# Kernel optimization log

Hardware: AMD Instinct MI355X
Metric: run time of the kernel (lower is better)

Reference implementation:

```python
import jax, jax.numpy as jnp
import numpy as np

SEQ_LEN, BATCH, T = 128, 32, 32
START, END = 30, 31  # start_tag / end_tag from init_kwargs


def setup_inputs() -> dict:
    key = jax.random.key(0)
    k1, k2 = jax.random.split(key)
    scores = jax.random.normal(k1, (SEQ_LEN, BATCH, T, T, T), dtype=jnp.float32)
    target = jax.random.randint(k2, (SEQ_LEN, BATCH, 1), 0, T ** 3, dtype=jnp.int64)
    mask = jnp.ones((SEQ_LEN, BATCH), dtype=bool)
    return {"scores": scores, "target": target, "mask": mask}


def reference(scores, target, mask):
    seq_len, bat = scores.shape[0], scores.shape[1]

    # gold-path energy: gather flattened tag-triple score at each step, masked sum
    flat = scores.reshape(seq_len, bat, -1)                  # (S, B, T^3)
    tg = jnp.take_along_axis(flat, target, axis=2)[..., 0]   # (S, B)
    tg_energy = jnp.sum(jnp.where(mask, tg, jnp.zeros((), tg.dtype)))

    # init partition over (prev_prev=START fixed out) -> (B, T, T) over (prev, cur)
    p1 = scores[0, :, START, START, :]                       # (B, T)
    partition = p1[:, :, None] + scores[1, :, START, :, :]   # (B, T, T)

    # forward-algorithm recurrence: logsumexp out oldest tag each step
    def step(part, inp):
        s_t, m_t = inp                                       # (B,T,T,T), (B,)
        cur = s_t + part[:, :, :, None]                      # broadcast over new tag
        cp = jax.nn.logsumexp(cur, axis=1)                   # (B, T, T)
        part = jnp.where(m_t[:, None, None], cp, part)
        return part, None

    partition, _ = jax.lax.scan(step, partition, (scores[2:], mask[2:]))

    z = partition[:, END, END].sum()
    return (z - tg_energy) / bat  # average_batch=True
```

## Files before the change

kernel.cpp:

```cpp
#include <hip/hip_runtime.h>
#include <hip/hip_bf16.h>
#include <math.h>

#define SEQ_LEN 128
#define BATCH   32
#define T       32
#define TT      (T*T)
#define TTT     (T*T*T)
#define START   30
#define END     31

#define LOG2E   1.44269504088896f
#define OFF4    5.77078016355587f

typedef unsigned long long u64;

__device__ __forceinline__ u64 pt_pack(int tag, float v) {
    union { float f; unsigned int u; } c; c.f = v;
    return ((u64)(unsigned int)tag << 32) | (u64)c.u;
}
__device__ __forceinline__ float pt_val(u64 w) {
    union { unsigned int u; float f; } c; c.u = (unsigned int)w; return c.f;
}
__device__ __forceinline__ int pt_tag(u64 w) { return (int)(w >> 32); }

__device__ __forceinline__ u64 ald64(const u64* p) {
    return __hip_atomic_load(p, __ATOMIC_RELAXED, __HIP_MEMORY_SCOPE_AGENT);
}
__device__ __forceinline__ void ast64(u64* p, u64 v) {
    __hip_atomic_store(p, v, __ATOMIC_RELAXED, __HIP_MEMORY_SCOPE_AGENT);
}

#define BLOCK_SYNC() do {                                   \
    asm volatile("s_waitcnt lgkmcnt(0)" ::: "memory");      \
    __builtin_amdgcn_sched_barrier(0);                      \
    __builtin_amdgcn_s_barrier();                           \
    __builtin_amdgcn_sched_barrier(0);                      \
} while (0)

__global__ __launch_bounds__(256) void tg_kernel(const float* __restrict__ scores,
                                                 const int*   __restrict__ target,
                                                 const int*   __restrict__ mask,
                                                 float*       __restrict__ ws) {
    int idx = blockIdx.x * 256 + threadIdx.x;
    float v = 0.0f;
    if (mask[idx] != 0) v = scores[(size_t)idx * TTT + target[idx]];
    #pragma unroll
    for (int off = 32; off > 0; off >>= 1) v += __shfl_down(v, off, 64);
    __shared__ float partial[4];
    int wave = threadIdx.x >> 6, lane = threadIdx.x & 63;
    if (lane == 0) partial[wave] = v;
    __syncthreads();
    if (threadIdx.x == 0)
        ws[blockIdx.x] = partial[0] + partial[1] + partial[2] + partial[3];
}

__global__ __launch_bounds__(256) void init_dfb(const float* __restrict__ scores,
                                                u64* __restrict__ ptF,
                                                u64* __restrict__ ptB) {
    const int blk = blockIdx.x, tid = threadIdx.x;
    if (blk < BATCH) {
        const int b = blk;
        u64* pt = ptF + (size_t)b * 2048;
        #pragma unroll
        for (int q = 0; q < 4; ++q) {
            int e = q * 256 + tid;
            int i = e & 31, j = e >> 5;
            float p1 = scores[(size_t)(0*BATCH + b)*TTT + START*TT + START*T + i];
            float s1 = scores[(size_t)(1*BATCH + b)*TTT + START*TT + i*T + j];
            pt[1024 + e] = pt_pack(1, __expf(p1 + s1));
            pt[e]        = 0ULL;
        }
    } else {
        const int b = blk - BATCH;
        u64* pt = ptB + (size_t)b * 2048;
        #pragma unroll
        for (int q = 0; q < 4; ++q) {
            int e = q * 256 + tid;
            float v = (e == END*T + END) ? 1.0f : 0.0f;
            pt[e]        = pt_pack(128, v);
            pt[1024 + e] = 0ULL;
        }
    }
}

__global__ __launch_bounds__(512, 4) void scan_rd(const float* __restrict__ scores,
                                                  const int*   __restrict__ maskI,
                                                  u64*         __restrict__ ptF,
                                                  u64*         __restrict__ ptB) {
    const int bid   = blockIdx.x;
    const int g     = bid & 7;
    const int chain = bid >> 3;
    const int b     = chain & 31;
    const bool dirB = (chain >> 5) != 0;
    const int tid   = threadIdx.x;
    const int lane  = tid & 63;

    const u64 mlo = __ballot(maskI[lane * BATCH + b] != 0);
    const u64 mhi = __ballot(maskI[(64 + lane) * BATCH + b] != 0);
    auto act_of = [&](int t) {
        return (((t < 64) ? (mlo >> t) : (mhi >> (t - 64))) & 1ULL) != 0ULL;
    };

    u64* const pt = (dirB ? ptB : ptF) + (size_t)b * 2048;
    const int i0 = tid >> 5;
    const int f  = tid & 31;
    const size_t offA = (size_t)i0 * TT + g * 128 + f * 4;
    auto sb = [&](int t) { return scores + ((size_t)t * BATCH + b) * TTT; };

    if (!dirB) {
        __shared__ __align__(16) float sm[4][128 * 33];
        __shared__ __align__(16) float pld[2][128];
        const int oF = tid >> 2, s4 = tid & 3;
        const int jj = oF >> 5, k = oF & 31;
        const int jcol = 4 * g + jj;
        const int ownW = k * 32 + jcol;
        float lastval = pt_val(pt[1024 + ownW]);

        float4 X0, X1;
        auto issue = [&](int t) {
            const float* p = sb(t) + offA;
            X0 = *(const float4*)p; X1 = *(const float4*)(p + 16 * TT);
        };
        auto scat = [&](int bf) {
            #pragma unroll
            for (int q = 0; q < 4; ++q) {
                sm[bf][(f*4 + q)*33 + i0]      = (&X0.x)[q];
                sm[bf][(f*4 + q)*33 + i0 + 16] = (&X1.x)[q];
            }
        };

        issue(2); scat(2);
        issue(3); scat(3);
        issue(4);
        __syncthreads();

        for (int t = 2; t <= 64; ++t) {
            const bool act  = act_of(t);
            const int  pbuf = t & 1;
            if (t + 2 <= 64) scat((t + 2) & 3);
            if (t + 3 <= 64) issue(t + 3);
            if (tid < 64) {
                const int tagw = t - 1;
                const u64* src = pt + (size_t)((t - 1) & 1) * 1024 + 128 * g;
                u64 w0, w1; bool d0 = false, d1 = false;
                for (;;) {
                    if (!d0) { w0 = ald64(src + lane);      d0 = pt_tag(w0) == tagw; }
                    if (!d1) { w1 = ald64(src + 64 + lane); d1 = pt_tag(w1) == tagw; }
                    if (__all(d0 && d1)) break;
                }
                pld[pbuf][lane]      = pt_val(w0);
                pld[pbuf][lane + 64] = pt_val(w1);
            }
            BLOCK_SYNC();
            u64* dst = pt + (size_t)(t & 1) * 1024;
            if (act) {
                const float* row = &sm[t & 3][oF * 33 + 8 * s4];
                const float* pp  = &pld[pbuf][jj * 32 + 8 * s4];
                float acc = 0.f;
                #pragma unroll
                for (int m = 0; m < 8; ++m)
                    acc = fmaf(exp2f(fmaf(row[m], LOG2E, -OFF4)), pp[m], acc);
                acc += __shfl_xor(acc, 1, 64);
                acc += __shfl_xor(acc, 2, 64);
                if (s4 == 0) { lastval = acc; ast64(dst + ownW, pt_pack(t, acc)); }
            } else {
                if (s4 == 0) ast64(dst + ownW, pt_pack(t, lastval));
            }
        }
    } else {
        __shared__ __align__(16) float pld[2][128];
        const int jj = f >> 3, k4 = f & 7;
        const int jb = 4 * g + jj;
        const int ownW0 = i0 * 32 + jb, ownW1 = (i0 + 16) * 32 + jb;
        float last0 = pt_val(pt[ownW0]);
        float last1 = pt_val(pt[ownW1]);

        float4 A0, A1, B0, B1;
        auto issueR = [&](float4& Y0, float4& Y1, int t) {
            const float* p = sb(t) + offA;
            Y0 = *(const float4*)p; Y1 = *(const float4*)(p + 16 * TT);
        };

        auto stepB = [&](int t, const float4& X0, const float4& X1) {
            const bool act  = act_of(t);
            const int  pbuf = t & 1;
            if (tid < 64) {
                const int tagw = t + 1;
                const u64* src = pt + (size_t)((t + 1) & 1) * 1024 + 128 * g;
                u64 w0, w1; bool d0 = false, d1 = false;
                for (;;) {
                    if (!d0) { w0 = ald64(src + lane);      d0 = pt_tag(w0) == tagw; }
                    if (!d1) { w1 = ald64(src + 64 + lane); d1 = pt_tag(w1) == tagw; }
                    if (__all(d0 && d1)) break;
                }
                pld[pbuf][lane]      = pt_val(w0);
                pld[pbuf][lane + 64] = pt_val(w1);
            }
            BLOCK_SYNC();
            u64* dst = pt + (size_t)(t & 1) * 1024;
            if (act) {
                const float4 Rv = *(const float4*)&pld[pbuf][jj * 32 + 4 * k4];
                float a0, a1;
                a0 = exp2f(fmaf(X0.x, LOG2E, -OFF4)) * Rv.x;
                a0 = fmaf(exp2f(fmaf(X0.y, LOG2E, -OFF4)), Rv.y, a0);
                a0 = fmaf(exp2f(fmaf(X0.z, LOG2E, -OFF4)), Rv.z, a0);
                a0 = fmaf(exp2f(fmaf(X0.w, LOG2E, -OFF4)), Rv.w, a0);
                a1 = exp2f(fmaf(X1.x, LOG2E, -OFF4)) * Rv.x;
                a1 = fmaf(exp2f(fmaf(X1.y, LOG2E, -OFF4)), Rv.y, a1);
                a1 = fmaf(exp2f(fmaf(X1.z, LOG2E, -OFF4)), Rv.z, a1);
                a1 = fmaf(exp2f(fmaf(X1.w, LOG2E, -OFF4)), Rv.w, a1);
                a0 += __shfl_xor(a0, 1, 64); a0 += __shfl_xor(a0, 2, 64); a0 += __shfl_xor(a0, 4, 64);
                a1 += __shfl_xor(a1, 1, 64); a1 += __shfl_xor(a1, 2, 64); a1 += __shfl_xor(a1, 4, 64);
                if (k4 == 0) {
                    last0 = a0; last1 = a1;
                    ast64(dst + ownW0, pt_pack(t, a0));
                    ast64(dst + ownW1, pt_pack(t, a1));
                }
            } else {
                if (k4 == 0) {
                    ast64(dst + ownW0, pt_pack(t, last0));
                    ast64(dst + ownW1, pt_pack(t, last1));
                }
            }
        };

        issueR(A0, A1, 127);
        for (int t = 127; t >= 65; t -= 2) {
            if (t - 1 >= 65) issueR(B0, B1, t - 1);
            stepB(t, A0, A1);
            if (t - 2 >= 65) issueR(A0, A1, t - 2);
            if (t - 1 >= 65) stepB(t - 1, B0, B1);
        }
    }
}

__global__ __launch_bounds__(1024) void finalize_dfb(const float* __restrict__ ws,
                                                     const u64*  __restrict__ ptF,
                                                     const u64*  __restrict__ ptB,
                                                     const int*  __restrict__ mask,
                                                     float*      __restrict__ out) {
    __shared__ float zs[32];
    const int w = threadIdx.x >> 6, lane = threadIdx.x & 63;
    for (int rep = 0; rep < 2; ++rep) {
        const int b = w + rep * 16;
        const u64* qf = ptF + (size_t)b * 2048;
        const u64* rb = ptB + (size_t)b * 2048 + 1024;
        float dot = 0.f;
        #pragma unroll
        for (int e = 0; e < 16; ++e) {
            const int x = lane + 64 * e;
            dot += pt_val(qf[x]) * pt_val(rb[(x & 31) * 32 + (x >> 5)]);
        }
        float cnt = 0.f;
        {
            int t = 2 + lane;
            if (t < SEQ_LEN) cnt += (mask[t*BATCH + b] != 0) ? 1.f : 0.f;
            t += 64;
            if (t < SEQ_LEN) cnt += (mask[t*BATCH + b] != 0) ? 1.f : 0.f;
        }
        #pragma unroll
        for (int off = 32; off > 0; off >>= 1) {
            dot += __shfl_xor(dot, off, 64);
            cnt += __shfl_xor(cnt, off, 64);
        }
        if (lane == 0) zs[b] = 4.0f * cnt + logf(dot);
    }
    __syncthreads();
    if (threadIdx.x == 0) {
        float tg = 0.f, z = 0.f;
        #pragma unroll
        for (int i = 0; i < 16; ++i) tg += ws[i];
        #pragma unroll
        for (int i = 0; i < 32; ++i) z += zs[i];
        out[0] = (z - tg) / (float)BATCH;
    }
}

__global__ __launch_bounds__(1024) void scan_fast(const float* __restrict__ scores,
                                                  const int*   __restrict__ maskI,
                                                  float*       __restrict__ ws) {
    const int b    = blockIdx.x;
    const int tid  = threadIdx.x;
    const int w    = tid >> 6;
    const int lane = tid & 63;
    const int h    = lane >> 4;
    const int jp   = (lane >> 3) & 1;
    const int k4   = lane & 7;
    const int j    = w * 2 + jp;

    __shared__ float Q[2][TT];
    __shared__ int   lmask[SEQ_LEN];
    if (tid < SEQ_LEN) lmask[tid] = maskI[tid * BATCH + b];
    {
        int x = tid >> 5, y = tid & 31;
        float p1 = scores[(size_t)(0*BATCH + b)*TTT + START*TT + START*T + x];
        float s1 = scores[(size_t)(1*BATCH + b)*TTT + START*TT + x*T + y];
        Q[1][x*T + y] = __expf(p1 + s1);
    }
    __syncthreads();
    const int loff = h*8*TT + j*T + k4*4;
    float4 SA[8], SB[8];
    auto issue = [&](float4 (&S)[8], int t) {
        const float* p = scores + ((size_t)t*BATCH + b)*TTT + loff;
        #pragma unroll
        for (int m = 0; m < 8; ++m) S[m] = *(const float4*)(p + m*TT);
    };
    auto process = [&](float4 (&S)[8], int t) {
        const float* qc = Q[(t-1) & 1];
        float*       qn = Q[t & 1];
        #pragma unroll
        for (int m = 0; m < 8; ++m) {
            S[m].x = exp2f(fmaf(S[m].x, LOG2E, -OFF4));
            S[m].y = exp2f(fmaf(S[m].y, LOG2E, -OFF4));
            S[m].z = exp2f(fmaf(S[m].z, LOG2E, -OFF4));
            S[m].w = exp2f(fmaf(S[m].w, LOG2E, -OFF4));
        }
        float4 acc = make_float4(0.f, 0.f, 0.f, 0.f);
        #pragma unroll
        for (int m = 0; m < 8; ++m) {
            float q = qc[(h*8 + m)*T + j];
            acc.x = fmaf(S[m].x, q, acc.x);
            acc.y = fmaf(S[m].y, q, acc.y);
            acc.z = fmaf(S[m].z, q, acc.z);
            acc.w = fmaf(S[m].w, q, acc.w);
        }
        acc.x += __shfl_xor(acc.x, 16, 64); acc.y += __shfl_xor(acc.y, 16, 64);
        acc.z += __shfl_xor(acc.z, 16, 64); acc.w += __shfl_xor(acc.w, 16, 64);
        acc.x += __shfl_xor(acc.x, 32, 64); acc.y += __shfl_xor(acc.y, 32, 64);
        acc.z += __shfl_xor(acc.z, 32, 64); acc.w += __shfl_xor(acc.w, 32, 64);
        if (lane < 16) {
            if (lmask[t] != 0) *(float4*)&qn[j*T + k4*4] = acc;
            else               *(float4*)&qn[j*T + k4*4] = *(const float4*)&qc[j*T + k4*4];
        }
        asm volatile("s_waitcnt lgkmcnt(0)" ::: "memory");
        __builtin_amdgcn_s_barrier();
    };
    issue(SA, 2);
    for (int t = 2; t < SEQ_LEN; t += 2) {
        issue(SB, t + 1);
        process(SA, t);
        if (t + 2 < SEQ_LEN) issue(SA, t + 2);
        process(SB, t + 1);
    }
    if (tid == 0) {
        int cnt = 0;
        for (int t = 2; t < SEQ_LEN; ++t) cnt += (lmask[t] != 0);
        ws[16 + b] = 4.0f * (float)cnt + logf(Q[1][END*T + END]);
    }
}

__global__ void finalize_simple(const float* __restrict__ ws, float* __restrict__ out) {
    if (threadIdx.x == 0) {
        float tg = 0.f, z = 0.f;
        #pragma unroll
        for (int i = 0; i < 16; ++i) tg += ws[i];
        #pragma unroll
        for (int i = 0; i < 32; ++i) z += ws[16 + i];
        out[0] = (z - tg) / (float)BATCH;
    }
}

extern "C" void kernel_launch(void* const* d_in, const int* in_sizes, int n_in,
                              void* d_out, int out_size, void* d_ws, size_t ws_size,
                              hipStream_t stream) {
    const float* scores = (const float*)d_in[0];
    const int*   target = (const int*)d_in[1];
    const int*   mask   = (const int*)d_in[2];
    float* out = (float*)d_out;
    float* ws  = (float*)d_ws;
    u64*   ptF = (u64*)((char*)d_ws + 1024);
    u64*   ptB = ptF + (size_t)BATCH * 2048;
    const size_t need = 1024 + (size_t)2 * BATCH * 2048 * sizeof(u64);

    tg_kernel<<<16, 256, 0, stream>>>(scores, target, mask, ws);
    if (ws_size >= need) {
        init_dfb<<<2*BATCH, 256, 0, stream>>>(scores, ptF, ptB);
        scan_rd<<<512, 512, 0, stream>>>(scores, mask, ptF, ptB);
        finalize_dfb<<<1, 1024, 0, stream>>>(ws, ptF, ptB, mask, out);
    } else {
        scan_fast<<<BATCH, 1024, 0, stream>>>(scores, mask, ws);
        finalize_simple<<<1, 64, 0, stream>>>(ws, out);
    }
}
```

Measured before the change: 185.6 us.

## Warp-specialize scan: producer waves prefetch exp'd scores, one consumer wave computes

Restructures the scan kernel into warp-specialized roles. Seven producer waves load scores, apply the exp transform and stage them in a 4-deep LDS ring. A single consumer wave polls the cross-block partition handoff, does the 32-term dot products and publishes results. Block-wide s_barrier syncs are replaced with LDS counters (readyCtr/doneGen) and spin-waits, so loads for future steps overlap the serial chain, and the forward and backward directions share one code path. The cost is that all per-step math lands on one wave, plus the risk of spin contention and ordering bugs under relaxed atomics.

Measured after the change: 200.5 us. +8.0%, slower.

```diff
diff --git a/kernel.cpp b/kernel.cpp
--- a/kernel.cpp
+++ b/kernel.cpp
@@ -9,6 +9,8 @@
 #define TTT     (T*T*T)
 #define START   30
 #define END     31
+#define NGEN    63
+#define TSTR    36
 
 #define LOG2E   1.44269504088896f
 #define OFF4    5.77078016355587f
@@ -31,10 +33,8 @@
     __hip_atomic_store(p, v, __ATOMIC_RELAXED, __HIP_MEMORY_SCOPE_AGENT);
 }
 
-#define BLOCK_SYNC() do {                                   \
+#define LGKM0_FENCE() do {                                  \
     asm volatile("s_waitcnt lgkmcnt(0)" ::: "memory");      \
-    __builtin_amdgcn_sched_barrier(0);                      \
-    __builtin_amdgcn_s_barrier();                           \
     __builtin_amdgcn_sched_barrier(0);                      \
 } while (0)
 
@@ -84,7 +84,7 @@
     }
 }
 
-__global__ __launch_bounds__(512, 4) void scan_rd(const float* __restrict__ scores,
+__global__ __launch_bounds__(512, 4) void scan_w0(const float* __restrict__ scores,
                                                   const int*   __restrict__ maskI,
                                                   u64*         __restrict__ ptF,
                                                   u64*         __restrict__ ptB) {
@@ -96,141 +96,124 @@
     const int tid   = threadIdx.x;
     const int lane  = tid & 63;
 
+    __shared__ __align__(16) float sm[4][128 * TSTR];
+    __shared__ float pldL[128];
+    __shared__ int readyCtr;
+    __shared__ int doneGen;
+
     const u64 mlo = __ballot(maskI[lane * BATCH + b] != 0);
     const u64 mhi = __ballot(maskI[(64 + lane) * BATCH + b] != 0);
     auto act_of = [&](int t) {
         return (((t < 64) ? (mlo >> t) : (mhi >> (t - 64))) & 1ULL) != 0ULL;
     };
 
+    if (tid == 0) { readyCtr = 0; doneGen = -1; }
+    __syncthreads();
+
     u64* const pt = (dirB ? ptB : ptF) + (size_t)b * 2048;
-    const int i0 = tid >> 5;
-    const int f  = tid & 31;
-    const size_t offA = (size_t)i0 * TT + g * 128 + f * 4;
     auto sb = [&](int t) { return scores + ((size_t)t * BATCH + b) * TTT; };
 
-    if (!dirB) {
-        __shared__ __align__(16) float sm[4][128 * 33];
-        __shared__ __align__(16) float pld[2][128];
-        const int oF = tid >> 2, s4 = tid & 3;
-        const int jj = oF >> 5, k = oF & 31;
-        const int jcol = 4 * g + jj;
-        const int ownW = k * 32 + jcol;
-        float lastval = pt_val(pt[1024 + ownW]);
-
-        float4 X0, X1;
-        auto issue = [&](int t) {
-            const float* p = sb(t) + offA;
-            X0 = *(const float4*)p; X1 = *(const float4*)(p + 16 * TT);
-        };
-        auto scat = [&](int bf) {
-            #pragma unroll
-            for (int q = 0; q < 4; ++q) {
-                sm[bf][(f*4 + q)*33 + i0]      = (&X0.x)[q];
-                sm[bf][(f*4 + q)*33 + i0 + 16] = (&X1.x)[q];
+    if (tid >= 64) {
+        const int u = tid - 64;
+        for (int gen = 0; gen < NGEN; ++gen) {
+            const int t = dirB ? (127 - gen) : (2 + gen);
+            if (gen >= 4) {
+                while (__hip_atomic_load(&doneGen, __ATOMIC_RELAXED,
+                                         __HIP_MEMORY_SCOPE_WORKGROUP) < gen - 4) {}
+                asm volatile("" ::: "memory");
+                __builtin_amdgcn_sched_barrier(0);
             }
-        };
-
-        issue(2); scat(2);
-        issue(3); scat(3);
-        issue(4);
-        __syncthreads();
-
-        for (int t = 2; t <= 64; ++t) {
-            const bool act  = act_of(t);
-            const int  pbuf = t & 1;
-            if (t + 2 <= 64) scat((t + 2) & 3);
-            if (t + 3 <= 64) issue(t + 3);
-            if (tid < 64) {
-                const int tagw = t - 1;
-                const u64* src = pt + (size_t)((t - 1) & 1) * 1024 + 128 * g;
-                u64 w0, w1; bool d0 = false, d1 = false;
-                for (;;) {
-                    if (!d0) { w0 = ald64(src + lane);      d0 = pt_tag(w0) == tagw; }
-                    if (!d1) { w1 = ald64(src + 64 + lane); d1 = pt_tag(w1) == tagw; }
-                    if (__all(d0 && d1)) break;
+            const int buf = gen & 3;
+            if (act_of(t)) {
+                const float* base = sb(t);
+                for (int p = u; p < 1024; p += 448) {
+                    const int i = p >> 5;
+                    const int c = p & 31;
+                    float4 v = *(const float4*)(base + (size_t)i * TT + g * 128 + c * 4);
+                    v.x = exp2f(fmaf(v.x, LOG2E, -OFF4));
+                    v.y = exp2f(fmaf(v.y, LOG2E, -OFF4));
+                    v.z = exp2f(fmaf(v.z, LOG2E, -OFF4));
+                    v.w = exp2f(fmaf(v.w, LOG2E, -OFF4));
+                    if (!dirB) {
+                        const int r0 = c * 4;
+                        sm[buf][(r0 + 0) * TSTR + i] = v.x;
+                        sm[buf][(r0 + 1) * TSTR + i] = v.y;
+                        sm[buf][(r0 + 2) * TSTR + i] = v.z;
+                        sm[buf][(r0 + 3) * TSTR + i] = v.w;
+                    } else {
+                        const int row = i * 4 + (c >> 3);
+                        const int col = (c & 7) * 4;
+                        *(float4*)&sm[buf][row * TSTR + col] = v;
+                    }
                 }
-                pld[pbuf][lane]      = pt_val(w0);
-                pld[pbuf][lane + 64] = pt_val(w1);
             }
-            BLOCK_SYNC();
+            LGKM0_FENCE();
+            if (lane == 0)
+                __hip_atomic_fetch_add(&readyCtr, 1, __ATOMIC_RELAXED,
+                                       __HIP_MEMORY_SCOPE_WORKGROUP);
+        }
+    } else {
+        const int o0 = lane, o1 = lane + 64;
+        int w0own, w1own, p0off, p1off;
+        if (!dirB) {
+            const int k = lane & 31;
+            const int jj0 = lane >> 5, jj1 = 2 + (lane >> 5);
+            w0own = k * 32 + 4 * g + jj0;
+            w1own = k * 32 + 4 * g + jj1;
+            p0off = jj0 * 32; p1off = jj1 * 32;
+        } else {
+            w0own = (o0 >> 2) * 32 + 4 * g + (o0 & 3);
+            w1own = (o1 >> 2) * 32 + 4 * g + (o1 & 3);
+            p0off = (o0 & 3) * 32; p1off = (o1 & 3) * 32;
+        }
+        const int parInit = dirB ? 0 : 1;
+        float last0 = pt_val(pt[parInit * 1024 + w0own]);
+        float last1 = pt_val(pt[parInit * 1024 + w1own]);
+
+        for (int gen = 0; gen < NGEN; ++gen) {
+            const int t    = dirB ? (127 - gen) : (2 + gen);
+            const bool act = act_of(t);
+            const int buf  = gen & 3;
+            const int tagw = dirB ? (t + 1) : (t - 1);
+            const int spar = dirB ? ((t + 1) & 1) : ((t - 1) & 1);
+
+            const u64* src = pt + (size_t)spar * 1024 + 128 * g;
+            u64 a0, a1; bool d0 = false, d1 = false;
+            for (;;) {
+                if (!d0) { a0 = ald64(src + lane);      d0 = pt_tag(a0) == tagw; }
+                if (!d1) { a1 = ald64(src + 64 + lane); d1 = pt_tag(a1) == tagw; }
+                if (__all(d0 && d1)) break;
+            }
+
             u64* dst = pt + (size_t)(t & 1) * 1024;
             if (act) {
-                const float* row = &sm[t & 3][oF * 33 + 8 * s4];
-                const float* pp  = &pld[pbuf][jj * 32 + 8 * s4];
-                float acc = 0.f;
+                pldL[lane]      = pt_val(a0);
+                pldL[lane + 64] = pt_val(a1);
+                while (__hip_atomic_load(&readyCtr, __ATOMIC_RELAXED,
+                                         __HIP_MEMORY_SCOPE_WORKGROUP) < 7 * (gen + 1)) {}
+                asm volatile("" ::: "memory");
+                LGKM0_FENCE();
+                const float* e0 = &sm[buf][o0 * TSTR];
+                const float* e1 = &sm[buf][o1 * TSTR];
+                const float* p0 = &pldL[p0off];
+                const float* p1 = &pldL[p1off];
+                float acc0 = 0.f, acc1 = 0.f;
                 #pragma unroll
-                for (int m = 0; m < 8; ++m)
-                    acc = fmaf(exp2f(fmaf(row[m], LOG2E, -OFF4)), pp[m], acc);
-                acc += __shfl_xor(acc, 1, 64);
-                acc += __shfl_xor(acc, 2, 64);
-                if (s4 == 0) { lastval = acc; ast64(dst + ownW, pt_pack(t, acc)); }
+                for (int m = 0; m < 32; ++m) {
+                    acc0 = fmaf(e0[m], p0[m], acc0);
+                    acc1 = fmaf(e1[m], p1[m], acc1);
+                }
+                last0 = acc0; last1 = acc1;
+                ast64(dst + w0own, pt_pack(t, acc0));
+                ast64(dst + w1own, pt_pack(t, acc1));
             } else {
-                if (s4 == 0) ast64(dst + ownW, pt_pack(t, lastval));
+                ast64(dst + w0own, pt_pack(t, last0));
+                ast64(dst + w1own, pt_pack(t, last1));
             }
-        }
-    } else {
-        __shared__ __align__(16) float pld[2][128];
-        const int jj = f >> 3, k4 = f & 7;
-        const int jb = 4 * g + jj;
-        const int ownW0 = i0 * 32 + jb, ownW1 = (i0 + 16) * 32 + jb;
-        float last0 = pt_val(pt[ownW0]);
-        float last1 = pt_val(pt[ownW1]);
-
-        float4 A0, A1, B0, B1;
-        auto issueR = [&](float4& Y0, float4& Y1, int t) {
-            const float* p = sb(t) + offA;
-            Y0 = *(const float4*)p; Y1 = *(const float4*)(p + 16 * TT);
-        };
-
-        auto stepB = [&](int t, const float4& X0, const float4& X1) {
-            const bool act  = act_of(t);
-            const int  pbuf = t & 1;
-            if (tid < 64) {
-                const int tagw = t + 1;
-                const u64* src = pt + (size_t)((t + 1) & 1) * 1024 + 128 * g;
-                u64 w0, w1; bool d0 = false, d1 = false;
-                for (;;) {
-                    if (!d0) { w0 = ald64(src + lane);      d0 = pt_tag(w0) == tagw; }
-                    if (!d1) { w1 = ald64(src + 64 + lane); d1 = pt_tag(w1) == tagw; }
-                    if (__all(d0 && d1)) break;
-                }
-                pld[pbuf][lane]      = pt_val(w0);
-                pld[pbuf][lane + 64] = pt_val(w1);
-            }
-            BLOCK_SYNC();
-            u64* dst = pt + (size_t)(t & 1) * 1024;
-            if (act) {
-                const float4 Rv = *(const float4*)&pld[pbuf][jj * 32 + 4 * k4];
-                float a0, a1;
-                a0 = exp2f(fmaf(X0.x, LOG2E, -OFF4)) * Rv.x;
-                a0 = fmaf(exp2f(fmaf(X0.y, LOG2E, -OFF4)), Rv.y, a0);
-                a0 = fmaf(exp2f(fmaf(X0.z, LOG2E, -OFF4)), Rv.z, a0);
-                a0 = fmaf(exp2f(fmaf(X0.w, LOG2E, -OFF4)), Rv.w, a0);
-                a1 = exp2f(fmaf(X1.x, LOG2E, -OFF4)) * Rv.x;
-                a1 = fmaf(exp2f(fmaf(X1.y, LOG2E, -OFF4)), Rv.y, a1);
-                a1 = fmaf(exp2f(fmaf(X1.z, LOG2E, -OFF4)), Rv.z, a1);
-                a1 = fmaf(exp2f(fmaf(X1.w, LOG2E, -OFF4)), Rv.w, a1);
-                a0 += __shfl_xor(a0, 1, 64); a0 += __shfl_xor(a0, 2, 64); a0 += __shfl_xor(a0, 4, 64);
-                a1 += __shfl_xor(a1, 1, 64); a1 += __shfl_xor(a1, 2, 64); a1 += __shfl_xor(a1, 4, 64);
-                if (k4 == 0) {
-                    last0 = a0; last1 = a1;
-                    ast64(dst + ownW0, pt_pack(t, a0));
-                    ast64(dst + ownW1, pt_pack(t, a1));
-                }
-            } else {
-                if (k4 == 0) {
-                    ast64(dst + ownW0, pt_pack(t, last0));
-                    ast64(dst + ownW1, pt_pack(t, last1));
-                }
-            }
-        };
-
-        issueR(A0, A1, 127);
-        for (int t = 127; t >= 65; t -= 2) {
-            if (t - 1 >= 65) issueR(B0, B1, t - 1);
-            stepB(t, A0, A1);
-            if (t - 2 >= 65) issueR(A0, A1, t - 2);
-            if (t - 1 >= 65) stepB(t - 1, B0, B1);
+            LGKM0_FENCE();
+            if (lane == 0)
+                __hip_atomic_store(&doneGen, gen, __ATOMIC_RELAXED,
+                                   __HIP_MEMORY_SCOPE_WORKGROUP);
         }
     }
 }
@@ -376,7 +359,7 @@
     tg_kernel<<<16, 256, 0, stream>>>(scores, target, mask, ws);
     if (ws_size >= need) {
         init_dfb<<<2*BATCH, 256, 0, stream>>>(scores, ptF, ptB);
-        scan_rd<<<512, 512, 0, stream>>>(scores, mask, ptF, ptB);
+        scan_w0<<<512, 512, 0, stream>>>(scores, mask, ptF, ptB);
         finalize_dfb<<<1, 1024, 0, stream>>>(ws, ptF, ptB, mask, out);
     } else {
         scan_fast<<<BATCH, 1024, 0, stream>>>(scores, mask, ws);
```

## Add mirrored fast-path exchange buffers and remap blocks for cross-block polling

Applied to the files above, without the earlier changes.

Each published step value is now written twice: a plain store to a mirrored buffer and an agent-scope atomic store to the original buffer. Consumers poll the mirror with sc0 loads first and fall back to atomic loads, aiming to cut cross-block handoff latency in the inter-block recurrence. The block-index mapping also changes from grouping the 8 slices of a chain together to interleaving chains across slices, which changes how cooperating blocks are placed across XCDs/CUs. The cost is extra stores and workspace, and the mirror path depends on cache-coherence behaviour of sc0 loads.

Result: slower. 204.8 us (+10.4%).

```diff
diff --git a/kernel.cpp b/kernel.cpp
--- a/kernel.cpp
+++ b/kernel.cpp
@@ -29,6 +29,17 @@
 }
 __device__ __forceinline__ void ast64(u64* p, u64 v) {
     __hip_atomic_store(p, v, __ATOMIC_RELAXED, __HIP_MEMORY_SCOPE_AGENT);
+}
+
+__device__ __forceinline__ void st_plain(u64* p, u64 v) {
+    asm volatile("global_store_dwordx2 %0, %1, off" :: "v"(p), "v"(v) : "memory");
+}
+__device__ __forceinline__ void ld_fast2(const u64* p0, const u64* p1,
+                                         u64& r0, u64& r1) {
+    asm volatile("global_load_dwordx2 %0, %2, off sc0\n\t"
+                 "global_load_dwordx2 %1, %3, off sc0\n\t"
+                 "s_waitcnt vmcnt(0)"
+                 : "=&v"(r0), "=&v"(r1) : "v"(p0), "v"(p1) : "memory");
 }
 
 #define BLOCK_SYNC() do {                                   \
@@ -57,40 +68,48 @@
 
 __global__ __launch_bounds__(256) void init_dfb(const float* __restrict__ scores,
                                                 u64* __restrict__ ptF,
-                                                u64* __restrict__ ptB) {
+                                                u64* __restrict__ ptB,
+                                                u64* __restrict__ ftF,
+                                                u64* __restrict__ ftB) {
     const int blk = blockIdx.x, tid = threadIdx.x;
     if (blk < BATCH) {
         const int b = blk;
         u64* pt = ptF + (size_t)b * 2048;
+        u64* ft = ftF + (size_t)b * 2048;
         #pragma unroll
         for (int q = 0; q < 4; ++q) {
             int e = q * 256 + tid;
             int i = e & 31, j = e >> 5;
             float p1 = scores[(size_t)(0*BATCH + b)*TTT + START*TT + START*T + i];
             float s1 = scores[(size_t)(1*BATCH + b)*TTT + START*TT + i*T + j];
-            pt[1024 + e] = pt_pack(1, __expf(p1 + s1));
-            pt[e]        = 0ULL;
+            u64 w = pt_pack(1, __expf(p1 + s1));
+            pt[1024 + e] = w;  ft[1024 + e] = w;
+            pt[e]        = 0ULL;  ft[e] = 0ULL;
         }
     } else {
         const int b = blk - BATCH;
         u64* pt = ptB + (size_t)b * 2048;
+        u64* ft = ftB + (size_t)b * 2048;
         #pragma unroll
         for (int q = 0; q < 4; ++q) {
             int e = q * 256 + tid;
             float v = (e == END*T + END) ? 1.0f : 0.0f;
-            pt[e]        = pt_pack(128, v);
-            pt[1024 + e] = 0ULL;
-        }
-    }
-}
-
-__global__ __launch_bounds__(512, 4) void scan_rd(const float* __restrict__ scores,
-                                                  const int*   __restrict__ maskI,
-                                                  u64*         __restrict__ ptF,
-                                                  u64*         __restrict__ ptB) {
+            u64 w = pt_pack(128, v);
+            pt[e] = w;  ft[e] = w;
+            pt[1024 + e] = 0ULL;  ft[1024 + e] = 0ULL;
+        }
+    }
+}
+
+__global__ __launch_bounds__(512, 4) void scan_xl2(const float* __restrict__ scores,
+                                                   const int*   __restrict__ maskI,
+                                                   u64*         __restrict__ ptF,
+                                                   u64*         __restrict__ ptB,
+                                                   u64*         __restrict__ ftF,
+                                                   u64*         __restrict__ ftB) {
     const int bid   = blockIdx.x;
-    const int g     = bid & 7;
-    const int chain = bid >> 3;
+    const int chain = bid & 63;
+    const int g     = bid >> 6;
     const int b     = chain & 31;
     const bool dirB = (chain >> 5) != 0;
     const int tid   = threadIdx.x;
@@ -103,10 +122,27 @@
     };
 
     u64* const pt = (dirB ? ptB : ptF) + (size_t)b * 2048;
+    u64* const ft = (dirB ? ftB : ftF) + (size_t)b * 2048;
     const int i0 = tid >> 5;
     const int f  = tid & 31;
     const size_t offA = (size_t)i0 * TT + g * 128 + f * 4;
     auto sb = [&](int t) { return scores + ((size_t)t * BATCH + b) * TTT; };
+
+    auto poll128 = [&](int spar, int tagw, u64& w0, u64& w1) {
+        const u64* src  = pt + (size_t)spar * 1024 + 128 * g;
+        const u64* fsrc = ft + (size_t)spar * 1024 + 128 * g;
+        bool d0 = false, d1 = false;
+        for (;;) {
+            u64 f0, f1;
+            ld_fast2(fsrc + lane, fsrc + 64 + lane, f0, f1);
+            if (!d0 && pt_tag(f0) == tagw) { w0 = f0; d0 = true; }
+            if (!d1 && pt_tag(f1) == tagw) { w1 = f1; d1 = true; }
+            if (__all(d0 && d1)) break;
+            if (!d0) { u64 x = ald64(src + lane);      if (pt_tag(x) == tagw) { w0 = x; d0 = true; } }
+            if (!d1) { u64 x = ald64(src + 64 + lane); if (pt_tag(x) == tagw) { w1 = x; d1 = true; } }
+            if (__all(d0 && d1)) break;
+        }
+    };
 
     if (!dirB) {
         __shared__ __align__(16) float sm[4][128 * 33];
@@ -141,19 +177,14 @@
             if (t + 2 <= 64) scat((t + 2) & 3);
             if (t + 3 <= 64) issue(t + 3);
             if (tid < 64) {
-                const int tagw = t - 1;
-                const u64* src = pt + (size_t)((t - 1) & 1) * 1024 + 128 * g;
-                u64 w0, w1; bool d0 = false, d1 = false;
-                for (;;) {
-                    if (!d0) { w0 = ald64(src + lane);      d0 = pt_tag(w0) == tagw; }
-                    if (!d1) { w1 = ald64(src + 64 + lane); d1 = pt_tag(w1) == tagw; }
-                    if (__all(d0 && d1)) break;
-                }
+                u64 w0, w1;
+                poll128((t - 1) & 1, t - 1, w0, w1);
                 pld[pbuf][lane]      = pt_val(w0);
                 pld[pbuf][lane + 64] = pt_val(w1);
             }
             BLOCK_SYNC();
-            u64* dst = pt + (size_t)(t & 1) * 1024;
+            u64* dst  = pt + (size_t)(t & 1) * 1024;
+            u64* fdst = ft + (size_t)(t & 1) * 1024;
             if (act) {
                 const float* row = &sm[t & 3][oF * 33 + 8 * s4];
                 const float* pp  = &pld[pbuf][jj * 32 + 8 * s4];
@@ -163,9 +194,18 @@
                     acc = fmaf(exp2f(fmaf(row[m], LOG2E, -OFF4)), pp[m], acc);
                 acc += __shfl_xor(acc, 1, 64);
                 acc += __shfl_xor(acc, 2, 64);
-                if (s4 == 0) { lastval = acc; ast64(dst + ownW, pt_pack(t, acc)); }
+                if (s4 == 0) {
+                    lastval = acc;
+                    u64 w = pt_pack(t, acc);
+                    st_plain(fdst + ownW, w);
+                    ast64(dst + ownW, w);
+                }
             } else {
-                if (s4 == 0) ast64(dst + ownW, pt_pack(t, lastval));
+                if (s4 == 0) {
+                    u64 w = pt_pack(t, lastval);
+                    st_plain(fdst + ownW, w);
+                    ast64(dst + ownW, w);
+                }
             }
         }
     } else {
@@ -186,19 +226,14 @@
             const bool act  = act_of(t);
             const int  pbuf = t & 1;
             if (tid < 64) {
-                const int tagw = t + 1;
-                const u64* src = pt + (size_t)((t + 1) & 1) * 1024 + 128 * g;
-                u64 w0, w1; bool d0 = false, d1 = false;
-                for (;;) {
-                    if (!d0) { w0 = ald64(src + lane);      d0 = pt_tag(w0) == tagw; }
-                    if (!d1) { w1 = ald64(src + 64 + lane); d1 = pt_tag(w1) == tagw; }
-                    if (__all(d0 && d1)) break;
-                }
+                u64 w0, w1;
+                poll128((t + 1) & 1, t + 1, w0, w1);
                 pld[pbuf][lane]      = pt_val(w0);
                 pld[pbuf][lane + 64] = pt_val(w1);
             }
             BLOCK_SYNC();
-            u64* dst = pt + (size_t)(t & 1) * 1024;
+            u64* dst  = pt + (size_t)(t & 1) * 1024;
+            u64* fdst = ft + (size_t)(t & 1) * 1024;
             if (act) {
                 const float4 Rv = *(const float4*)&pld[pbuf][jj * 32 + 4 * k4];
                 float a0, a1;
@@ -214,13 +249,15 @@
                 a1 += __shfl_xor(a1, 1, 64); a1 += __shfl_xor(a1, 2, 64); a1 += __shfl_xor(a1, 4, 64);
                 if (k4 == 0) {
                     last0 = a0; last1 = a1;
-                    ast64(dst + ownW0, pt_pack(t, a0));
-                    ast64(dst + ownW1, pt_pack(t, a1));
+                    u64 wA = pt_pack(t, a0), wB = pt_pack(t, a1);
+                    st_plain(fdst + ownW0, wA);  ast64(dst + ownW0, wA);
+                    st_plain(fdst + ownW1, wB);  ast64(dst + ownW1, wB);
                 }
             } else {
                 if (k4 == 0) {
-                    ast64(dst + ownW0, pt_pack(t, last0));
-                    ast64(dst + ownW1, pt_pack(t, last1));
+                    u64 wA = pt_pack(t, last0), wB = pt_pack(t, last1);
+                    st_plain(fdst + ownW0, wA);  ast64(dst + ownW0, wA);
+                    st_plain(fdst + ownW1, wB);  ast64(dst + ownW1, wB);
                 }
             }
         };
@@ -371,12 +408,14 @@
     float* ws  = (float*)d_ws;
     u64*   ptF = (u64*)((char*)d_ws + 1024);
     u64*   ptB = ptF + (size_t)BATCH * 2048;
-    const size_t need = 1024 + (size_t)2 * BATCH * 2048 * sizeof(u64);
+    u64*   ftF = ptB + (size_t)BATCH * 2048;
+    u64*   ftB = ftF + (size_t)BATCH * 2048;
+    const size_t need = 1024 + (size_t)4 * BATCH * 2048 * sizeof(u64);
 
     tg_kernel<<<16, 256, 0, stream>>>(scores, target, mask, ws);
     if (ws_size >= need) {
-        init_dfb<<<2*BATCH, 256, 0, stream>>>(scores, ptF, ptB);
-        scan_rd<<<512, 512, 0, stream>>>(scores, mask, ptF, ptB);
+        init_dfb<<<2*BATCH, 256, 0, stream>>>(scores, ptF, ptB, ftF, ftB);
+        scan_xl2<<<512, 512, 0, stream>>>(scores, mask, ptF, ptB, ftF, ftB);
         finalize_dfb<<<1, 1024, 0, stream>>>(ws, ptF, ptB, mask, out);
     } else {
         scan_fast<<<BATCH, 1024, 0, stream>>>(scores, mask, ws);
```

## Pair consecutive time steps per cross-block exchange to halve global handoffs

Applied to the files above, without the earlier changes.

The forward and backward chains now advance two time steps per published exchange (32 hops instead of ~63), keeping the intermediate step in shared memory and only publishing every second partition. Each block polls the whole 1024-entry partition instead of a 128-entry slice, and layouts are transposed so the second step's operand lines up with block ownership. This removes half of the global atomic poll/publish round-trips on the serial critical path, but adds an extra block barrier and more per-hop polling traffic and loads.

Result: slower. 266.7 us (+43.7%).

```diff
diff --git a/kernel.cpp b/kernel.cpp
--- a/kernel.cpp
+++ b/kernel.cpp
@@ -9,6 +9,7 @@
 #define TTT     (T*T*T)
 #define START   30
 #define END     31
+#define NHOP    32
 
 #define LOG2E   1.44269504088896f
 #define OFF4    5.77078016355587f
@@ -55,9 +56,9 @@
         ws[blockIdx.x] = partial[0] + partial[1] + partial[2] + partial[3];
 }
 
-__global__ __launch_bounds__(256) void init_dfb(const float* __restrict__ scores,
-                                                u64* __restrict__ ptF,
-                                                u64* __restrict__ ptB) {
+__global__ __launch_bounds__(256) void init_pf(const float* __restrict__ scores,
+                                               u64* __restrict__ ptF,
+                                               u64* __restrict__ ptB) {
     const int blk = blockIdx.x, tid = threadIdx.x;
     if (blk < BATCH) {
         const int b = blk;
@@ -65,11 +66,11 @@
         #pragma unroll
         for (int q = 0; q < 4; ++q) {
             int e = q * 256 + tid;
-            int i = e & 31, j = e >> 5;
+            int i = e >> 5, j = e & 31;
             float p1 = scores[(size_t)(0*BATCH + b)*TTT + START*TT + START*T + i];
             float s1 = scores[(size_t)(1*BATCH + b)*TTT + START*TT + i*T + j];
-            pt[1024 + e] = pt_pack(1, __expf(p1 + s1));
-            pt[e]        = 0ULL;
+            pt[e]        = pt_pack(0, __expf(p1 + s1));
+            pt[1024 + e] = 0ULL;
         }
     } else {
         const int b = blk - BATCH;
@@ -77,14 +78,13 @@
         #pragma unroll
         for (int q = 0; q < 4; ++q) {
             int e = q * 256 + tid;
-            float v = (e == END*T + END) ? 1.0f : 0.0f;
-            pt[e]        = pt_pack(128, v);
+            pt[e]        = pt_pack(0, (e == END*T + END) ? 1.0f : 0.0f);
             pt[1024 + e] = 0ULL;
         }
     }
 }
 
-__global__ __launch_bounds__(512, 4) void scan_rd(const float* __restrict__ scores,
+__global__ __launch_bounds__(512, 4) void scan_pf(const float* __restrict__ scores,
                                                   const int*   __restrict__ maskI,
                                                   u64*         __restrict__ ptF,
                                                   u64*         __restrict__ ptB) {
@@ -94,163 +94,205 @@
     const int b     = chain & 31;
     const bool dirB = (chain >> 5) != 0;
     const int tid   = threadIdx.x;
-    const int lane  = tid & 63;
-
-    const u64 mlo = __ballot(maskI[lane * BATCH + b] != 0);
-    const u64 mhi = __ballot(maskI[(64 + lane) * BATCH + b] != 0);
+
+    __shared__ __align__(16) float sm[2][128 * 33];
+    __shared__ float pldP[32 * 33];
+    __shared__ float Ild[136];
+
+    const u64 mlo = __ballot(maskI[(tid & 63) * BATCH + b] != 0);
+    const u64 mhi = __ballot(maskI[(64 + (tid & 63)) * BATCH + b] != 0);
     auto act_of = [&](int t) {
         return (((t < 64) ? (mlo >> t) : (mhi >> (t - 64))) & 1ULL) != 0ULL;
     };
 
     u64* const pt = (dirB ? ptB : ptF) + (size_t)b * 2048;
-    const int i0 = tid >> 5;
-    const int f  = tid & 31;
-    const size_t offA = (size_t)i0 * TT + g * 128 + f * 4;
     auto sb = [&](int t) { return scores + ((size_t)t * BATCH + b) * TTT; };
 
+    const int out = tid >> 2, s = tid & 3;
+
+    auto getmode = [&](int p, int& md, int& tA, int& tB) {
+        if (!dirB) {
+            if (p == 31) { md = act_of(64) ? 1 : 0; tA = 64; tB = 64; return; }
+            int t0 = 2 + 2*p, t1 = t0 + 1;
+            bool a0 = act_of(t0), a1 = act_of(t1);
+            if (a0 && a1)      { md = 2; tA = t0; tB = t1; }
+            else if (a0 || a1) { md = 1; tA = a0 ? t0 : t1; tB = tA; }
+            else               { md = 0; tA = t0; tB = t1; }
+        } else {
+            if (p == 31) { md = act_of(65) ? 1 : 0; tA = 65; tB = 65; return; }
+            int th = 127 - 2*p, tl = th - 1;
+            bool ah = act_of(th), al = act_of(tl);
+            if (ah && al)      { md = 2; tA = th; tB = tl; }
+            else if (ah || al) { md = 1; tA = ah ? th : tl; tB = tA; }
+            else               { md = 0; tA = th; tB = tl; }
+        }
+    };
+
+    auto poll = [&](int p) {
+        const u64* src = pt + (size_t)(p & 1) * 1024;
+        const int x0 = 2 * tid;
+        u64 a0v, a1v; bool d0 = false, d1 = false;
+        for (;;) {
+            if (!d0) { a0v = ald64(src + x0);     d0 = pt_tag(a0v) == p; }
+            if (!d1) { a1v = ald64(src + x0 + 1); d1 = pt_tag(a1v) == p; }
+            if (__all(d0 && d1)) break;
+        }
+        const int u = x0 >> 5, v = x0 & 31;
+        pldP[u*33 + v]     = pt_val(a0v);
+        pldP[u*33 + v + 1] = pt_val(a1v);
+    };
+
     if (!dirB) {
-        __shared__ __align__(16) float sm[4][128 * 33];
-        __shared__ __align__(16) float pld[2][128];
-        const int oF = tid >> 2, s4 = tid & 3;
-        const int jj = oF >> 5, k = oF & 31;
-        const int jcol = 4 * g + jj;
-        const int ownW = k * 32 + jcol;
-        float lastval = pt_val(pt[1024 + ownW]);
-
-        float4 X0, X1;
-        auto issue = [&](int t) {
-            const float* p = sb(t) + offA;
-            X0 = *(const float4*)p; X1 = *(const float4*)(p + 16 * TT);
+        const int il = tid >> 5;
+        const int jl = tid & 31;
+        const size_t e0off = (size_t)il * TT + jl * T + 4 * g;
+        const int j1 = out >> 2, kq1 = out & 3;
+        const int kq2 = out >> 5, l2 = out & 31;
+
+        float4 c0, c1;
+        auto issueE0 = [&](int t) {
+            const float* p = sb(t) + e0off;
+            c0 = *(const float4*)p;
+            c1 = *(const float4*)(p + 16 * TT);
         };
-        auto scat = [&](int bf) {
+        auto scat = [&](int buf) {
             #pragma unroll
             for (int q = 0; q < 4; ++q) {
-                sm[bf][(f*4 + q)*33 + i0]      = (&X0.x)[q];
-                sm[bf][(f*4 + q)*33 + i0 + 16] = (&X1.x)[q];
+                sm[buf][(jl*4 + q)*33 + il]      = (&c0.x)[q];
+                sm[buf][(jl*4 + q)*33 + il + 16] = (&c1.x)[q];
             }
         };
-
-        issue(2); scat(2);
-        issue(3); scat(3);
-        issue(4);
+        float e1r[8];
+        auto issueE1 = [&](int t) {
+            const float* p = sb(t) + (size_t)(8*s) * TT + (4*g + kq2) * T + l2;
+            #pragma unroll
+            for (int q = 0; q < 8; ++q) e1r[q] = p[(size_t)q * TT];
+        };
+
+        int md, tA, tB;
+        getmode(0, md, tA, tB);
+        issueE0(tA); scat(0);
+        { int m2, a2, b2; getmode(1, m2, a2, b2); issueE0(a2); }
         __syncthreads();
 
-        for (int t = 2; t <= 64; ++t) {
-            const bool act  = act_of(t);
-            const int  pbuf = t & 1;
-            if (t + 2 <= 64) scat((t + 2) & 3);
-            if (t + 3 <= 64) issue(t + 3);
-            if (tid < 64) {
-                const int tagw = t - 1;
-                const u64* src = pt + (size_t)((t - 1) & 1) * 1024 + 128 * g;
-                u64 w0, w1; bool d0 = false, d1 = false;
-                for (;;) {
-                    if (!d0) { w0 = ald64(src + lane);      d0 = pt_tag(w0) == tagw; }
-                    if (!d1) { w1 = ald64(src + 64 + lane); d1 = pt_tag(w1) == tagw; }
-                    if (__all(d0 && d1)) break;
+        for (int p = 0; p < NHOP; ++p) {
+            getmode(p, md, tA, tB);
+            if (p + 1 < NHOP) scat((p + 1) & 1);
+            if (p + 2 < NHOP) { int m2, a2, b2; getmode(p + 2, m2, a2, b2); issueE0(a2); }
+            issueE1(tB);
+            poll(p);
+            BLOCK_SYNC();
+            u64* dst = pt + (size_t)((p + 1) & 1) * 1024;
+            const int tg2 = p + 1;
+            if (md != 0) {
+                const float* row = &sm[p & 1][out * 33 + 8 * s];
+                float acc = 0.f;
+                #pragma unroll
+                for (int q = 0; q < 8; ++q)
+                    acc = fmaf(exp2f(fmaf(row[q], LOG2E, -OFF4)),
+                               pldP[(8*s + q)*33 + j1], acc);
+                acc += __shfl_xor(acc, 1, 64);
+                acc += __shfl_xor(acc, 2, 64);
+                if (s == 0) {
+                    if (md == 1) ast64(dst + j1*32 + 4*g + kq1, pt_pack(tg2, acc));
+                    else         Ild[out] = acc;
                 }
-                pld[pbuf][lane]      = pt_val(w0);
-                pld[pbuf][lane + 64] = pt_val(w1);
+            } else {
+                if (s == 0)
+                    ast64(dst + (4*g + kq2)*32 + l2,
+                          pt_pack(tg2, pldP[(4*g + kq2)*33 + l2]));
             }
             BLOCK_SYNC();
-            u64* dst = pt + (size_t)(t & 1) * 1024;
-            if (act) {
-                const float* row = &sm[t & 3][oF * 33 + 8 * s4];
-                const float* pp  = &pld[pbuf][jj * 32 + 8 * s4];
+            if (md == 2) {
                 float acc = 0.f;
                 #pragma unroll
-                for (int m = 0; m < 8; ++m)
-                    acc = fmaf(exp2f(fmaf(row[m], LOG2E, -OFF4)), pp[m], acc);
+                for (int q = 0; q < 8; ++q)
+                    acc = fmaf(exp2f(fmaf(e1r[q], LOG2E, -OFF4)),
+                               Ild[(8*s + q)*4 + kq2], acc);
                 acc += __shfl_xor(acc, 1, 64);
                 acc += __shfl_xor(acc, 2, 64);
-                if (s4 == 0) { lastval = acc; ast64(dst + ownW, pt_pack(t, acc)); }
+                if (s == 0) ast64(dst + (4*g + kq2)*32 + l2, pt_pack(tg2, acc));
+            }
+        }
+    } else {
+        const int i1 = out >> 5, jj = out & 31;
+        const int h2 = out & 31, iq2 = out >> 5;
+        float4 rh0, rh1, rl0, rl1;
+        auto issueEh = [&](int t) {
+            const float* p = sb(t) + (size_t)(4*g + i1) * TT + jj * T + 8 * s;
+            rh0 = *(const float4*)p; rh1 = *(const float4*)(p + 4);
+        };
+        auto issueEl = [&](int t) {
+            const float* p = sb(t) + (size_t)h2 * TT + (4*g + iq2) * T + 8 * s;
+            rl0 = *(const float4*)p; rl1 = *(const float4*)(p + 4);
+        };
+
+        for (int p = 0; p < NHOP; ++p) {
+            int md, tA, tB;
+            getmode(p, md, tA, tB);
+            issueEh(tA); issueEl(tB);
+            poll(p);
+            BLOCK_SYNC();
+            u64* dst = pt + (size_t)((p + 1) & 1) * 1024;
+            const int tg2 = p + 1;
+            if (md != 0) {
+                const float* pv = &pldP[jj*33 + 8*s];
+                float acc;
+                acc = exp2f(fmaf(rh0.x, LOG2E, -OFF4)) * pv[0];
+                acc = fmaf(exp2f(fmaf(rh0.y, LOG2E, -OFF4)), pv[1], acc);
+                acc = fmaf(exp2f(fmaf(rh0.z, LOG2E, -OFF4)), pv[2], acc);
+                acc = fmaf(exp2f(fmaf(rh0.w, LOG2E, -OFF4)), pv[3], acc);
+                acc = fmaf(exp2f(fmaf(rh1.x, LOG2E, -OFF4)), pv[4], acc);
+                acc = fmaf(exp2f(fmaf(rh1.y, LOG2E, -OFF4)), pv[5], acc);
+                acc = fmaf(exp2f(fmaf(rh1.z, LOG2E, -OFF4)), pv[6], acc);
+                acc = fmaf(exp2f(fmaf(rh1.w, LOG2E, -OFF4)), pv[7], acc);
+                acc += __shfl_xor(acc, 1, 64);
+                acc += __shfl_xor(acc, 2, 64);
+                if (s == 0) {
+                    if (md == 1) ast64(dst + (4*g + i1)*32 + jj, pt_pack(tg2, acc));
+                    else         Ild[i1*33 + jj] = acc;
+                }
             } else {
-                if (s4 == 0) ast64(dst + ownW, pt_pack(t, lastval));
-            }
-        }
-    } else {
-        __shared__ __align__(16) float pld[2][128];
-        const int jj = f >> 3, k4 = f & 7;
-        const int jb = 4 * g + jj;
-        const int ownW0 = i0 * 32 + jb, ownW1 = (i0 + 16) * 32 + jb;
-        float last0 = pt_val(pt[ownW0]);
-        float last1 = pt_val(pt[ownW1]);
-
-        float4 A0, A1, B0, B1;
-        auto issueR = [&](float4& Y0, float4& Y1, int t) {
-            const float* p = sb(t) + offA;
-            Y0 = *(const float4*)p; Y1 = *(const float4*)(p + 16 * TT);
-        };
-
-        auto stepB = [&](int t, const float4& X0, const float4& X1) {
-            const bool act  = act_of(t);
-            const int  pbuf = t & 1;
-            if (tid < 64) {
-                const int tagw = t + 1;
-                const u64* src = pt + (size_t)((t + 1) & 1) * 1024 + 128 * g;
-                u64 w0, w1; bool d0 = false, d1 = false;
-                for (;;) {
-                    if (!d0) { w0 = ald64(src + lane);      d0 = pt_tag(w0) == tagw; }
-                    if (!d1) { w1 = ald64(src + 64 + lane); d1 = pt_tag(w1) == tagw; }
-                    if (__all(d0 && d1)) break;
-                }
-                pld[pbuf][lane]      = pt_val(w0);
-                pld[pbuf][lane + 64] = pt_val(w1);
+                if (s == 0)
+                    ast64(dst + h2*32 + 4*g + iq2,
+                          pt_pack(tg2, pldP[h2*33 + 4*g + iq2]));
             }
             BLOCK_SYNC();
-            u64* dst = pt + (size_t)(t & 1) * 1024;
-            if (act) {
-                const float4 Rv = *(const float4*)&pld[pbuf][jj * 32 + 4 * k4];
-                float a0, a1;
-                a0 = exp2f(fmaf(X0.x, LOG2E, -OFF4)) * Rv.x;
-                a0 = fmaf(exp2f(fmaf(X0.y, LOG2E, -OFF4)), Rv.y, a0);
-                a0 = fmaf(exp2f(fmaf(X0.z, LOG2E, -OFF4)), Rv.z, a0);
-                a0 = fmaf(exp2f(fmaf(X0.w, LOG2E, -OFF4)), Rv.w, a0);
-                a1 = exp2f(fmaf(X1.x, LOG2E, -OFF4)) * Rv.x;
-                a1 = fmaf(exp2f(fmaf(X1.y, LOG2E, -OFF4)), Rv.y, a1);
-                a1 = fmaf(exp2f(fmaf(X1.z, LOG2E, -OFF4)), Rv.z, a1);
-                a1 = fmaf(exp2f(fmaf(X1.w, LOG2E, -OFF4)), Rv.w, a1);
-                a0 += __shfl_xor(a0, 1, 64); a0 += __shfl_xor(a0, 2, 64); a0 += __shfl_xor(a0, 4, 64);
-                a1 += __shfl_xor(a1, 1, 64); a1 += __shfl_xor(a1, 2, 64); a1 += __shfl_xor(a1, 4, 64);
-                if (k4 == 0) {
-                    last0 = a0; last1 = a1;
-                    ast64(dst + ownW0, pt_pack(t, a0));
-                    ast64(dst + ownW1, pt_pack(t, a1));
-                }
-            } else {
-                if (k4 == 0) {
-                    ast64(dst + ownW0, pt_pack(t, last0));
-                    ast64(dst + ownW1, pt_pack(t, last1));
-                }
+            if (md == 2) {
+                const float* iv = &Ild[iq2*33 + 8*s];
+                float acc;
+                acc = exp2f(fmaf(rl0.x, LOG2E, -OFF4)) * iv[0];
+                acc = fmaf(exp2f(fmaf(rl0.y, LOG2E, -OFF4)), iv[1], acc);
+                acc = fmaf(exp2f(fmaf(rl0.z, LOG2E, -OFF4)), iv[2], acc);
+                acc = fmaf(exp2f(fmaf(rl0.w, LOG2E, -OFF4)), iv[3], acc);
+                acc = fmaf(exp2f(fmaf(rl1.x, LOG2E, -OFF4)), iv[4], acc);
+                acc = fmaf(exp2f(fmaf(rl1.y, LOG2E, -OFF4)), iv[5], acc);
+                acc = fmaf(exp2f(fmaf(rl1.z, LOG2E, -OFF4)), iv[6], acc);
+                acc = fmaf(exp2f(fmaf(rl1.w, LOG2E, -OFF4)), iv[7], acc);
+                acc += __shfl_xor(acc, 1, 64);
+                acc += __shfl_xor(acc, 2, 64);
+                if (s == 0) ast64(dst + h2*32 + 4*g + iq2, pt_pack(tg2, acc));
             }
-        };
-
-        issueR(A0, A1, 127);
-        for (int t = 127; t >= 65; t -= 2) {
-            if (t - 1 >= 65) issueR(B0, B1, t - 1);
-            stepB(t, A0, A1);
-            if (t - 2 >= 65) issueR(A0, A1, t - 2);
-            if (t - 1 >= 65) stepB(t - 1, B0, B1);
-        }
-    }
-}
-
-__global__ __launch_bounds__(1024) void finalize_dfb(const float* __restrict__ ws,
-                                                     const u64*  __restrict__ ptF,
-                                                     const u64*  __restrict__ ptB,
-                                                     const int*  __restrict__ mask,
-                                                     float*      __restrict__ out) {
+        }
+    }
+}
+
+__global__ __launch_bounds__(1024) void finalize_pf(const float* __restrict__ ws,
+                                                    const u64*  __restrict__ ptF,
+                                                    const u64*  __restrict__ ptB,
+                                                    const int*  __restrict__ mask,
+                                                    float*      __restrict__ out) {
     __shared__ float zs[32];
     const int w = threadIdx.x >> 6, lane = threadIdx.x & 63;
     for (int rep = 0; rep < 2; ++rep) {
         const int b = w + rep * 16;
         const u64* qf = ptF + (size_t)b * 2048;
-        const u64* rb = ptB + (size_t)b * 2048 + 1024;
+        const u64* rb = ptB + (size_t)b * 2048;
         float dot = 0.f;
         #pragma unroll
         for (int e = 0; e < 16; ++e) {
             const int x = lane + 64 * e;
-            dot += pt_val(qf[x]) * pt_val(rb[(x & 31) * 32 + (x >> 5)]);
+            dot += pt_val(qf[x]) * pt_val(rb[x]);
         }
         float cnt = 0.f;
         {
@@ -375,9 +417,9 @@
 
     tg_kernel<<<16, 256, 0, stream>>>(scores, target, mask, ws);
     if (ws_size >= need) {
-        init_dfb<<<2*BATCH, 256, 0, stream>>>(scores, ptF, ptB);
-        scan_rd<<<512, 512, 0, stream>>>(scores, mask, ptF, ptB);
-        finalize_dfb<<<1, 1024, 0, stream>>>(ws, ptF, ptB, mask, out);
+        init_pf<<<2*BATCH, 256, 0, stream>>>(scores, ptF, ptB);
+        scan_pf<<<512, 512, 0, stream>>>(scores, mask, ptF, ptB);
+        finalize_pf<<<1, 1024, 0, stream>>>(ws, ptF, ptB, mask, out);
     } else {
         scan_fast<<<BATCH, 1024, 0, stream>>>(scores, mask, ws);
         finalize_simple<<<1, 64, 0, stream>>>(ws, out);
```
